# Kernel optimization log

Hardware: AMD Instinct MI355X
Metric: run time of the kernel (lower is better)

## Reference

```python
import jax, jax.numpy as jnp
import numpy as np

BEAM = 4
SOS = 1


def _gru_cell(x, h, Wih, Whh, bih, bhh):
    # x,h: [B,H]; Wih,Whh: [3H,H]; torch GRUCell math
    gi = x @ Wih.T + bih
    gh = h @ Whh.T + bhh
    ir, iz, inn = jnp.split(gi, 3, axis=-1)
    hr, hz, hn = jnp.split(gh, 3, axis=-1)
    r = jax.nn.sigmoid(ir + hr)
    z = jax.nn.sigmoid(iz + hz)
    n = jnp.tanh(inn + r * hn)
    return (1.0 - z) * n + z * h


def setup_inputs() -> dict:
    key = jax.random.key(0)
    V, H, S, L = 32000, 1024, 256, 48
    ks = jax.random.split(key, 10)
    p = lambda k, shape: (jax.random.normal(k, shape, jnp.float32) * 0.02)
    return {
        "input_seq": jax.random.randint(ks[0], (S, 1), 0, V),
        "input_length": S,
        "max_length": L,
        "emb": p(ks[1], (V, H)),
        "enc_Wih": p(ks[2], (3 * H, H)),
        "enc_Whh": p(ks[3], (3 * H, H)),
        "enc_bih": jnp.zeros((3 * H,), jnp.float32),
        "enc_bhh": jnp.zeros((3 * H,), jnp.float32),
        "dec_Wih": p(ks[4], (3 * H, H)),
        "dec_Whh": p(ks[5], (3 * H, H)),
        "dec_bih": jnp.zeros((3 * H,), jnp.float32),
        "dec_bhh": jnp.zeros((3 * H,), jnp.float32),
        "Wc": p(ks[6], (H, 2 * H)),
        "Wout": p(ks[7], (V, H)),
    }


def _beam_search(input_seq, max_length, emb, enc_Wih, enc_Whh, enc_bih, enc_bhh,
                 dec_Wih, dec_Whh, dec_bih, dec_bhh, Wc, Wout):
    H = emb.shape[1]
    # ---- encoder: single-layer GRU over [S] tokens ----
    seq_emb = emb[input_seq[:, 0]]  # [S,H]

    def enc_step(h, x):
        hn = _gru_cell(x[None, :], h, enc_Wih, enc_Whh, enc_bih, enc_bhh)
        return hn, hn[0]

    h0 = jnp.zeros((1, H), emb.dtype)
    h_final, enc_out = jax.lax.scan(enc_step, h0, seq_emb)  # enc_out: [S,H]

    # ---- beam state (all beams start from encoder final hidden, SOS token) ----
    h = jnp.tile(h_final, (BEAM, 1))            # [4,H]
    inputs = jnp.full((BEAM,), SOS, jnp.int32)  # [4]
    cum = jnp.zeros((BEAM,), emb.dtype)
    tokens = jnp.zeros((BEAM, max_length), jnp.int32)
    shist = jnp.zeros((BEAM, max_length), emb.dtype)

    def dec_step(carry, step):
        h, inputs, cum, tokens, shist = carry
        x = emb[inputs]                                     # [4,H]
        hnew = _gru_cell(x, h, dec_Wih, dec_Whh, dec_bih, dec_bhh)  # [4,H]
        # Luong dot attention over encoder outputs
        attn = jax.nn.softmax(jnp.einsum('sh,bh->bs', enc_out, hnew), axis=-1)
        ctx = attn @ enc_out                                # [4,H]
        concat = jnp.tanh(jnp.concatenate([hnew, ctx], axis=-1) @ Wc.T)
        logp = jax.nn.log_softmax(concat @ Wout.T, axis=-1)  # [4,V]
        tp, ti = jax.lax.top_k(logp, BEAM)                  # [4,4]
        # step 0: only beam 0 expands (all beams identical), as in original
        valid = jnp.where(step == 0, jnp.arange(BEAM) == 0,
                          jnp.ones((BEAM,), bool))
        cand = jnp.where(valid[:, None], cum[:, None] + tp, -jnp.inf).reshape(-1)
        sel_scores, sel = jax.lax.top_k(cand, BEAM)         # [4]
        bi = sel // BEAM   # parent beam index i
        jj = sel % BEAM    # topk column index j
        # Faithful to original bug: new hidden indexed by column j, not parent i
        new_h = hnew[jj]
        new_inputs = ti[bi, jj]
        step_scores = tp[bi, jj]
        new_tokens = tokens[bi].at[:, step].set(new_inputs)
        new_shist = shist[bi].at[:, step].set(step_scores)
        return (new_h, new_inputs, sel_scores, new_tokens, new_shist), None

    (h, inputs, cum, tokens, shist), _ = jax.lax.scan(
        dec_step, (h, inputs, cum, tokens, shist), jnp.arange(max_length))
    best = jnp.argmax(cum)  # all beams same length -> avg == cum ranking
    return tokens[best], shist[best]


def reference(input_seq, input_length, max_length, emb, enc_Wih, enc_Whh,
              enc_bih, enc_bhh, dec_Wih, dec_Whh, dec_bih, dec_bhh, Wc, Wout):
    # input_length: full sequence is used (original packs to input_length;
    # here input_length == seq_len)
    return _beam_search(input_seq, max_length, emb, enc_Wih, enc_Whh, enc_bih,
                        enc_bhh, dec_Wih, dec_Whh, dec_bih, dec_bhh, Wc, Wout)
```

## Files before the change

kernel.cpp:

```cpp
#include <hip/hip_runtime.h>
#include <hip/hip_bf16.h>

#define HDIM 1024
#define G3   3072
#define CHK  16
#define NEG_INF (-__builtin_inff())
#define EB   32

typedef unsigned short u16;
typedef unsigned int   u32;

__device__ __forceinline__ float bf2f(u32 h){ union{u32 u; float f;} t; t.u = h<<16; return t.f; }

__device__ __forceinline__ float wred_sum(float v){
  #pragma unroll
  for(int o=32;o;o>>=1) v += __shfl_xor(v,o,64);
  return v;
}
__device__ __forceinline__ float wred_max(float v){
  #pragma unroll
  for(int o=32;o;o>>=1) v = fmaxf(v,__shfl_xor(v,o,64));
  return v;
}

__device__ __forceinline__ void load16w(const void* W, long long eoff, int bf, float* x){
  if(bf){
    const uint4* q = (const uint4*)((const u16*)W + eoff);
    uint4 a = q[0], b = q[1];
    x[0]=bf2f(a.x&0xffffu); x[1]=bf2f(a.x>>16);
    x[2]=bf2f(a.y&0xffffu); x[3]=bf2f(a.y>>16);
    x[4]=bf2f(a.z&0xffffu); x[5]=bf2f(a.z>>16);
    x[6]=bf2f(a.w&0xffffu); x[7]=bf2f(a.w>>16);
    x[8]=bf2f(b.x&0xffffu); x[9]=bf2f(b.x>>16);
    x[10]=bf2f(b.y&0xffffu); x[11]=bf2f(b.y>>16);
    x[12]=bf2f(b.z&0xffffu); x[13]=bf2f(b.z>>16);
    x[14]=bf2f(b.w&0xffffu); x[15]=bf2f(b.w>>16);
  } else {
    const float4* q = (const float4*)((const float*)W + eoff);
    float4 A=q[0],B=q[1],C=q[2],D=q[3];
    x[0]=A.x;x[1]=A.y;x[2]=A.z;x[3]=A.w;
    x[4]=B.x;x[5]=B.y;x[6]=B.z;x[7]=B.w;
    x[8]=C.x;x[9]=C.y;x[10]=C.z;x[11]=C.w;
    x[12]=D.x;x[13]=D.y;x[14]=D.z;x[15]=D.w;
  }
}
__device__ __forceinline__ void load16f(const float* p, float* x){
  const float4* q=(const float4*)p;
  float4 A=q[0],B=q[1],C=q[2],D=q[3];
  x[0]=A.x;x[1]=A.y;x[2]=A.z;x[3]=A.w;
  x[4]=B.x;x[5]=B.y;x[6]=B.z;x[7]=B.w;
  x[8]=C.x;x[9]=C.y;x[10]=C.z;x[11]=C.w;
  x[12]=D.x;x[13]=D.y;x[14]=D.z;x[15]=D.w;
}
__device__ __forceinline__ float loadscal(const void* p, long long i, int bf){
  return bf ? bf2f(((const u16*)p)[i]) : ((const float*)p)[i];
}
__device__ __forceinline__ float sigf(float x){ return 1.f/(1.f+expf(-x)); }

__device__ __forceinline__ void dot4_accum(const float* w, const float xr[4][16], float a[4]){
  #pragma unroll
  for(int i=0;i<16;i++){
    a[0] += w[i]*xr[0][i];
    a[1] += w[i]*xr[1][i];
    a[2] += w[i]*xr[2][i];
    a[3] += w[i]*xr[3][i];
  }
}

__device__ __forceinline__ void insert4(float* v, int* ix, float nv, int ni){
  bool b3 = (nv>v[3]) || (nv==v[3] && ni<ix[3]);
  if(!b3) return;
  bool b2 = (nv>v[2]) || (nv==v[2] && ni<ix[2]);
  bool b1 = (nv>v[1]) || (nv==v[1] && ni<ix[1]);
  bool b0 = (nv>v[0]) || (nv==v[0] && ni<ix[0]);
  if(b0){ v[3]=v[2];ix[3]=ix[2]; v[2]=v[1];ix[2]=ix[1]; v[1]=v[0];ix[1]=ix[0]; v[0]=nv;ix[0]=ni; }
  else if(b1){ v[3]=v[2];ix[3]=ix[2]; v[2]=v[1];ix[2]=ix[1]; v[1]=nv;ix[1]=ni; }
  else if(b2){ v[3]=v[2];ix[3]=ix[2]; v[2]=nv;ix[2]=ni; }
  else { v[3]=nv; ix[3]=ni; }
}
__device__ __forceinline__ void merge4(const float* va, const int* ia, const float* vb, const int* ib, float* vo, int* io){
  int pa=0, pb=0;
  for(int k=0;k<4;k++){
    bool ta;
    if(pa>=4) ta=false;
    else if(pb>=4) ta=true;
    else ta = (va[pa]>vb[pb]) || (va[pa]==vb[pb] && ia[pa]<ib[pb]);
    if(ta){ vo[k]=va[pa]; io[k]=ia[pa]; pa++; }
    else  { vo[k]=vb[pb]; io[k]=ib[pb]; pb++; }
  }
}

__device__ __forceinline__ void gbar(int* cnt, int nblk, int it){
  __syncthreads();
  if(threadIdx.x==0){
    __hip_atomic_fetch_add(cnt, 1, __ATOMIC_ACQ_REL, __HIP_MEMORY_SCOPE_AGENT);
    int target = nblk*it;
    while(__hip_atomic_load(cnt, __ATOMIC_ACQUIRE, __HIP_MEMORY_SCOPE_AGENT) < target)
      __builtin_amdgcn_s_sleep(1);
  }
  __syncthreads();
  __builtin_amdgcn_fence(__ATOMIC_ACQUIRE, "agent");
}

__global__ __launch_bounds__(256) void k_probe(const u16* emb, int* flag, int* bar_cnt){
  __shared__ int cnt;
  if(threadIdx.x==0){ cnt=0; *bar_cnt=0; }
  __syncthreads();
  int c=0;
  for(int i=threadIdx.x;i<4096;i+=256){
    u32 e = (emb[i]>>7)&0xffu;
    if(e>=0x85u) c++;
  }
  atomicAdd(&cnt,c);
  __syncthreads();
  if(threadIdx.x==0) *flag = (cnt<100)?1:0;
}

__global__ __launch_bounds__(256) void k_enc_gi(const int* seq, const void* emb, const void* Wih,
                                                const void* bih, const int* flag, float* gi){
  int bf = *flag;
  int wg = blockIdx.x; int tg = wg>>3, rg = wg&7;
  int wave = threadIdx.x>>6, lane = threadIdx.x&63;
  int tok[4];
  #pragma unroll
  for(int j=0;j<4;j++) tok[j] = seq[tg*4+j];
  float xr[4][16];
  #pragma unroll
  for(int j=0;j<4;j++) load16w(emb, (long long)tok[j]*HDIM + lane*CHK, bf, xr[j]);
  for(int k=0;k<96;k++){
    int row = rg*384 + wave*96 + k;
    float w[16]; load16w(Wih, (long long)row*HDIM + lane*CHK, bf, w);
    float a[4]={0.f,0.f,0.f,0.f};
    dot4_accum(w, xr, a);
    float bias = loadscal(bih, row, bf);
    #pragma unroll
    for(int b=0;b<4;b++){
      float v = wred_sum(a[b]);
      if(lane==b) gi[(long long)(tg*4+b)*G3 + row] = v + bias;
    }
  }
}

__global__ __launch_bounds__(512,2) void k_enc_persist(const void* Whh, const void* bhh,
                                                       const int* flag, const float* gi,
                                                       float* enc_out, int S, int* bar_cnt){
  int bf = *flag;
  int wave = threadIdx.x>>6, lane = threadIdx.x&63;
  int dbase = blockIdx.x*32;
  __shared__ float gh_s[96];
  __shared__ float bhh_s[96];
  if(threadIdx.x<96){
    int rl = threadIdx.x;
    int row = (rl>>5)*HDIM + dbase + (rl&31);
    bhh_s[rl] = loadscal(bhh, row, bf);
  }
  float wreg[12][16];
  #pragma unroll
  for(int k=0;k<12;k++){
    int rl = wave*12 + k;
    int row = (rl>>5)*HDIM + dbase + (rl&31);
    load16w(Whh, (long long)row*HDIM + lane*CHK, bf, wreg[k]);
  }
  __syncthreads();

  for(int t=0;t<S;t++){
    if(t>0) gbar(bar_cnt, EB, t);
    float h[16];
    if(t>0){
      load16f(enc_out + (long long)(t-1)*HDIM + lane*CHK, h);
    } else {
      #pragma unroll
      for(int i=0;i<16;i++) h[i]=0.f;
    }
    #pragma unroll
    for(int k=0;k<12;k++){
      float a=0.f;
      #pragma unroll
      for(int i=0;i<16;i++) a += wreg[k][i]*h[i];
      a = wred_sum(a);
      if(lane==k) gh_s[wave*12+k] = a + bhh_s[wave*12+k];
    }
    __syncthreads();
    if(threadIdx.x<32){
      int d = threadIdx.x;
      int gd = dbase + d;
      const float* gir = gi + (long long)t*G3;
      float ir = gir[gd], iz = gir[HDIM+gd], in_ = gir[2*HDIM+gd];
      float hr = gh_s[d], hz = gh_s[32+d], hn = gh_s[64+d];
      float r = sigf(ir+hr);
      float z = sigf(iz+hz);
      float n = tanhf(in_ + r*hn);
      float hp = (t>0) ? enc_out[(long long)(t-1)*HDIM + gd] : 0.f;
      enc_out[(long long)t*HDIM + gd] = (1.f-z)*n + z*hp;
    }
  }
}

__global__ __launch_bounds__(256) void k_dec_init(const float* enc_out, int S, float* h_cur, float* cum,
                                                  int* cur_in, int* tokens, float* shist, int L){
  int t = threadIdx.x;
  const float* hf = enc_out + (long long)(S-1)*HDIM;
  for(int i=t;i<4*HDIM;i+=256) h_cur[i] = hf[i&(HDIM-1)];
  if(t<4){ cum[t]=0.f; cur_in[t]=1; }
  for(int i=t;i<4*L;i+=256){ tokens[i]=0; shist[i]=0.f; }
}

__global__ __launch_bounds__(256) void k_dec_gru(const void* emb, const void* Wih, const void* Whh,
                                                 const void* bih, const void* bhh, const int* flag,
                                                 const int* cur_in, const float* h_cur, float* hnew){
  int bf = *flag;
  __shared__ float gibuf[96], ghbuf[96];
  int wave = threadIdx.x>>6, lane = threadIdx.x&63;
  int base = blockIdx.x*8;
  float xr[4][16];
  int tok[4];
  #pragma unroll
  for(int b=0;b<4;b++) tok[b]=cur_in[b];
  #pragma unroll
  for(int b=0;b<4;b++) load16w(emb,(long long)tok[b]*HDIM+lane*CHK,bf,xr[b]);
  for(int k=0;k<6;k++){
    int idx = wave*6+k; int g = idx>>3, d = idx&7;
    int row = g*HDIM + base + d;
    float w[16]; load16w(Wih,(long long)row*HDIM+lane*CHK,bf,w);
    float a[4]={0.f,0.f,0.f,0.f};
    dot4_accum(w,xr,a);
    float bias = loadscal(bih,row,bf);
    #pragma unroll
    for(int b=0;b<4;b++){
      float v = wred_sum(a[b]);
      if(lane==b) gibuf[idx*4+b] = v + bias;
    }
  }
  #pragma unroll
  for(int b=0;b<4;b++) load16f(h_cur+(long long)b*HDIM+lane*CHK, xr[b]);
  for(int k=0;k<6;k++){
    int idx = wave*6+k; int g = idx>>3, d = idx&7;
    int row = g*HDIM + base + d;
    float w[16]; load16w(Whh,(long long)row*HDIM+lane*CHK,bf,w);
    float a[4]={0.f,0.f,0.f,0.f};
    dot4_accum(w,xr,a);
    float bias = loadscal(bhh,row,bf);
    #pragma unroll
    for(int b=0;b<4;b++){
      float v = wred_sum(a[b]);
      if(lane==b) ghbuf[idx*4+b] = v + bias;
    }
  }
  __syncthreads();
  if(threadIdx.x<32){
    int d = threadIdx.x&7, b = threadIdx.x>>3;
    float ir = gibuf[(0*8+d)*4+b], iz = gibuf[(1*8+d)*4+b], in_ = gibuf[(2*8+d)*4+b];
    float hr = ghbuf[(0*8+d)*4+b], hz = ghbuf[(1*8+d)*4+b], hn = ghbuf[(2*8+d)*4+b];
    float r = sigf(ir+hr);
    float z = sigf(iz+hz);
    float n = tanhf(in_ + r*hn);
    float h = h_cur[b*HDIM + base + d];
    hnew[b*HDIM + base + d] = (1.f-z)*n + z*h;
  }
}

__global__ __launch_bounds__(256) void k_dec_scores(const float* enc_out, const float* hnew, float* scores){
  int wave = threadIdx.x>>6, lane = threadIdx.x&63;
  float xr[4][16];
  #pragma unroll
  for(int b=0;b<4;b++) load16f(hnew+(long long)b*HDIM+lane*CHK, xr[b]);
  for(int k=0;k<4;k++){
    int s = (blockIdx.x*4+wave)*4+k;
    float w[16]; load16f(enc_out+(long long)s*HDIM+lane*CHK, w);
    float a[4]={0.f,0.f,0.f,0.f};
    dot4_accum(w,xr,a);
    #pragma unroll
    for(int b=0;b<4;b++){
      float v = wred_sum(a[b]);
      if(lane==b) scores[s*4+b] = v;
    }
  }
}

__global__ __launch_bounds__(256) void k_dec_attnctx(const float* enc_out, const float* scores_g,
                                                     float* ctx, int S){
  __shared__ float sc[256*4];
  int t = threadIdx.x;
  for(int i=t;i<S*4;i+=256) sc[i]=scores_g[i];
  __syncthreads();
  int wave = t>>6, lane = t&63;
  {
    int b = wave;
    float v[4];
    #pragma unroll
    for(int k=0;k<4;k++) v[k]=sc[(lane+64*k)*4+b];
    float m = fmaxf(fmaxf(v[0],v[1]),fmaxf(v[2],v[3]));
    m = wred_max(m);
    float e[4]; float ss=0.f;
    #pragma unroll
    for(int k=0;k<4;k++){ e[k]=expf(v[k]-m); ss+=e[k]; }
    ss = wred_sum(ss);
    #pragma unroll
    for(int k=0;k<4;k++) sc[(lane+64*k)*4+b] = e[k]/ss;
  }
  __syncthreads();
  int hl = t&127, bp = t>>7;
  int h = blockIdx.x*128 + hl;
  int b0 = bp*2;
  float a0=0.f, a1=0.f;
  for(int s=0;s<S;s++){
    float e = enc_out[(long long)s*HDIM + h];
    a0 += sc[s*4+b0]*e;
    a1 += sc[s*4+b0+1]*e;
  }
  ctx[b0*HDIM+h]=a0; ctx[(b0+1)*HDIM+h]=a1;
}

__global__ __launch_bounds__(256) void k_dec_wc(const void* Wc, const int* flag, const float* hnew,
                                                const float* ctx, float* concat){
  int bf = *flag;
  int wave = threadIdx.x>>6, lane = threadIdx.x&63;
  int r0 = blockIdx.x*16 + wave*4;
  float xr[4][16];
  #pragma unroll
  for(int b=0;b<4;b++) load16f(hnew+(long long)b*HDIM+lane*CHK, xr[b]);
  float acc[4][4];
  #pragma unroll
  for(int k=0;k<4;k++){
    #pragma unroll
    for(int b=0;b<4;b++) acc[k][b]=0.f;
  }
  #pragma unroll
  for(int k=0;k<4;k++){
    float w[16]; load16w(Wc,(long long)(r0+k)*2048 + lane*CHK, bf, w);
    #pragma unroll
    for(int i=0;i<16;i++){
      acc[k][0]+=w[i]*xr[0][i]; acc[k][1]+=w[i]*xr[1][i];
      acc[k][2]+=w[i]*xr[2][i]; acc[k][3]+=w[i]*xr[3][i];
    }
  }
  #pragma unroll
  for(int b=0;b<4;b++) load16f(ctx+(long long)b*HDIM+lane*CHK, xr[b]);
  #pragma unroll
  for(int k=0;k<4;k++){
    float w[16]; load16w(Wc,(long long)(r0+k)*2048 + 1024 + lane*CHK, bf, w);
    #pragma unroll
    for(int i=0;i<16;i++){
      acc[k][0]+=w[i]*xr[0][i]; acc[k][1]+=w[i]*xr[1][i];
      acc[k][2]+=w[i]*xr[2][i]; acc[k][3]+=w[i]*xr[3][i];
    }
  }
  #pragma unroll
  for(int k=0;k<4;k++){
    #pragma unroll
    for(int b=0;b<4;b++){
      float v = wred_sum(acc[k][b]);
      if(lane == k*4+b) concat[b*HDIM + r0 + k] = tanhf(v);
    }
  }
}

__global__ __launch_bounds__(512) void k_dec_logits(const void* Wout, const int* flag, const float* concat,
                                                    float* pm, float* ps, float* ptv, int* pti, int V){
  int bf = *flag;
  int wave = threadIdx.x>>6, lane = threadIdx.x&63;
  float xr[4][16];
  #pragma unroll
  for(int b=0;b<4;b++) load16f(concat+(long long)b*HDIM+lane*CHK, xr[b]);
  int wbase = blockIdx.x*125;
  int off  = (wave<5) ? wave*16 : 80 + (wave-5)*15;
  int cnt  = (wave<5) ? 16 : 15;
  float m[4], s[4], tv[4][4]; int ti_[4][4];
  #pragma unroll
  for(int b=0;b<4;b++){
    m[b]=NEG_INF; s[b]=0.f;
    #pragma unroll
    for(int j=0;j<4;j++){ tv[b][j]=NEG_INF; ti_[b][j]=0; }
  }
  for(int k=0;k<cnt;k++){
    int row = wbase + off + k;
    if(row>=V) break;
    float w[16]; load16w(Wout,(long long)row*HDIM+lane*CHK,bf,w);
    float a[4]={0.f,0.f,0.f,0.f};
    dot4_accum(w,xr,a);
    a[0]=wred_sum(a[0]); a[1]=wred_sum(a[1]); a[2]=wred_sum(a[2]); a[3]=wred_sum(a[3]);
    if(lane==0){
      #pragma unroll
      for(int b=0;b<4;b++){
        float v = a[b];
        if(v>m[b]){ s[b]=s[b]*expf(m[b]-v)+1.f; m[b]=v; }
        else s[b] += expf(v-m[b]);
        insert4(tv[b], ti_[b], v, row);
      }
    }
  }
  __shared__ float lm[32], lssum[32], ltv[128]; __shared__ int lti[128];
  if(lane==0){
    #pragma unroll
    for(int b=0;b<4;b++){
      lm[wave*4+b]=m[b]; lssum[wave*4+b]=s[b];
      #pragma unroll
      for(int j=0;j<4;j++){ ltv[(wave*4+b)*4+j]=tv[b][j]; lti[(wave*4+b)*4+j]=ti_[b][j]; }
    }
  }
  __syncthreads();
  if(threadIdx.x==0){
    for(int b=0;b<4;b++){
      float M=NEG_INF;
      for(int w=0;w<8;w++) M=fmaxf(M,lm[w*4+b]);
      float S=0.f;
      for(int w=0;w<8;w++) S += lssum[w*4+b]*expf(lm[w*4+b]-M);
      float cv[4]; int ci[4];
      for(int j=0;j<4;j++){ cv[j]=ltv[(0*4+b)*4+j]; ci[j]=lti[(0*4+b)*4+j]; }
      for(int w=1;w<8;w++){
        float vo[4]; int io[4];
        merge4(cv,ci,&ltv[(w*4+b)*4],&lti[(w*4+b)*4],vo,io);
        for(int j=0;j<4;j++){ cv[j]=vo[j]; ci[j]=io[j]; }
      }
      pm[blockIdx.x*4+b]=M; ps[blockIdx.x*4+b]=S;
      for(int j=0;j<4;j++){ ptv[(blockIdx.x*4+b)*4+j]=cv[j]; pti[(blockIdx.x*4+b)*4+j]=ci[j]; }
    }
  }
}

__global__ __launch_bounds__(256) void k_dec_finalize(const float* pm, const float* ps, const float* ptv,
                                                      const int* pti, const float* hnew, float* h_cur,
                                                      float* cum, int* cur_in, int* tokens, float* shist,
                                                      int step, int L, const int* flag, void* dout){
  __shared__ float red[256];
  __shared__ float tpv[4][4]; __shared__ int tpi[4][4];
  __shared__ float logZ[4];
  __shared__ float mtv[256*4]; __shared__ int mti[256*4];
  __shared__ int l_bi[4], l_jj[4], l_tok[4]; __shared__ float l_ss[4], l_cum[4];
  __shared__ int otok[4*64]; __shared__ float oshi[4*64];
  __shared__ int bbest;
  int t = threadIdx.x;

  for(int b=0;b<4;b++){
    float v = pm[t*4+b];
    red[t]=v; __syncthreads();
    for(int st=128;st;st>>=1){ if(t<st) red[t]=fmaxf(red[t],red[t+st]); __syncthreads(); }
    float M = red[0]; __syncthreads();
    red[t] = ps[t*4+b]*expf(v-M); __syncthreads();
    for(int st=128;st;st>>=1){ if(t<st) red[t]+=red[t+st]; __syncthreads(); }
    if(t==0) logZ[b]=M+logf(red[0]);
    __syncthreads();
  }
  for(int b=0;b<4;b++){
    for(int j=0;j<4;j++){ mtv[t*4+j]=ptv[(t*4+b)*4+j]; mti[t*4+j]=pti[(t*4+b)*4+j]; }
    __syncthreads();
    for(int st=1; st<256; st<<=1){
      if((t & (2*st-1))==0 && t+st<256){
        float vo[4]; int io[4];
        merge4(&mtv[t*4], &mti[t*4], &mtv[(t+st)*4], &mti[(t+st)*4], vo, io);
        for(int j=0;j<4;j++){ mtv[t*4+j]=vo[j]; mti[t*4+j]=io[j]; }
      }
      __syncthreads();
    }
    if(t<4){ tpv[b][t]=mtv[t]-logZ[b]; tpi[b][t]=mti[t]; }
    __syncthreads();
  }
  if(t==0){
    float oc[4];
    for(int b=0;b<4;b++) oc[b]=cum[b];
    float cand[16];
    for(int b=0;b<4;b++)
      for(int j=0;j<4;j++){
        bool valid = (step>0)||(b==0);
        cand[b*4+j] = valid ? oc[b]+tpv[b][j] : NEG_INF;
      }
    bool used[16];
    for(int i=0;i<16;i++) used[i]=false;
    for(int q=0;q<4;q++){
      int best=0; float bv=NEG_INF;
      for(int i=0;i<16;i++){ if(!used[i] && cand[i]>bv){ bv=cand[i]; best=i; } }
      used[best]=true;
      int bi = best>>2, jj = best&3;
      l_bi[q]=bi; l_jj[q]=jj; l_tok[q]=tpi[bi][jj]; l_ss[q]=tpv[bi][jj]; l_cum[q]=bv;
    }
  }
  __syncthreads();
  for(int i=t;i<4*L;i+=256){ otok[i]=tokens[i]; oshi[i]=shist[i]; }
  __syncthreads();
  for(int i=t;i<4*L;i+=256){
    int q=i/L, c=i%L;
    int src=l_bi[q];
    tokens[i] = (c==step)? l_tok[q] : otok[src*L+c];
    shist[i]  = (c==step)? l_ss[q]  : oshi[src*L+c];
  }
  if(t<4){ cum[t]=l_cum[t]; cur_in[t]=l_tok[t]; }
  for(int i=t;i<4*HDIM;i+=256){
    int q=i>>10;
    h_cur[i] = hnew[l_jj[q]*HDIM + (i&(HDIM-1))];
  }
  if(step==L-1){
    if(t==0){
      int bb=0; float bv=l_cum[0];
      for(int b=1;b<4;b++) if(l_cum[b]>bv){ bv=l_cum[b]; bb=b; }
      bbest=bb;
    }
    __syncthreads();
    int bb=bbest; int bf=*flag;
    for(int c=t;c<L;c+=256){
      float tokv = (float)((c==step)? l_tok[bb] : otok[l_bi[bb]*L+c]);
      float shv  = (c==step)? l_ss[bb] : oshi[l_bi[bb]*L+c];
      if(bf){
        __hip_bfloat16* o = (__hip_bfloat16*)dout;
        o[c]   = __float2bfloat16(tokv);
        o[L+c] = __float2bfloat16(shv);
      } else {
        float* o = (float*)dout;
        o[c]   = tokv;
        o[L+c] = shv;
      }
    }
  }
}

extern "C" void kernel_launch(void* const* d_in, const int* in_sizes, int n_in,
                              void* d_out, int out_size, void* d_ws, size_t ws_size,
                              hipStream_t stream) {
  const int* seq   = (const int*)d_in[0];
  const void* emb  = d_in[3];
  const void* eWih = d_in[4]; const void* eWhh = d_in[5];
  const void* ebih = d_in[6]; const void* ebhh = d_in[7];
  const void* dWih = d_in[8]; const void* dWhh = d_in[9];
  const void* dbih = d_in[10]; const void* dbhh = d_in[11];
  const void* Wc   = d_in[12]; const void* Wout = d_in[13];

  int S = in_sizes[0];
  int L = out_size/2;
  int V = in_sizes[13]/HDIM;

  char* p = (char*)d_ws;
  auto carve = [&](size_t bytes)->void* {
    void* r = (void*)p;
    p += (bytes + 255) & ~(size_t)255;
    return r;
  };
  int*   flag    = (int*)  carve(4);
  int*   bar_cnt = (int*)  carve(4);
  float* gi_enc  = (float*)carve((size_t)S*G3*4);
  float* enc_out = (float*)carve((size_t)S*HDIM*4);
  float* h_cur   = (float*)carve(4*HDIM*4);
  float* hnew    = (float*)carve(4*HDIM*4);
  float* scoresb = (float*)carve((size_t)S*4*4);
  float* ctx     = (float*)carve(4*HDIM*4);
  float* concat  = (float*)carve(4*HDIM*4);
  float* pm      = (float*)carve(256*4*4);
  float* ps      = (float*)carve(256*4*4);
  float* ptv     = (float*)carve(256*16*4);
  int*   pti     = (int*)  carve(256*16*4);
  float* cum     = (float*)carve(4*4);
  int*   cur_in  = (int*)  carve(4*4);
  int*   tokens  = (int*)  carve(4*L*4);
  float* shist   = (float*)carve(4*L*4);

  k_probe<<<1,256,0,stream>>>((const u16*)emb, flag, bar_cnt);
  k_enc_gi<<<(S/4)*8,256,0,stream>>>(seq, emb, eWih, ebih, flag, gi_enc);
  k_enc_persist<<<EB,512,0,stream>>>(eWhh, ebhh, flag, gi_enc, enc_out, S, bar_cnt);
  k_dec_init<<<1,256,0,stream>>>(enc_out, S, h_cur, cum, cur_in, tokens, shist, L);
  for(int st=0;st<L;st++){
    k_dec_gru<<<128,256,0,stream>>>(emb, dWih, dWhh, dbih, dbhh, flag, cur_in, h_cur, hnew);
    k_dec_scores<<<16,256,0,stream>>>(enc_out, hnew, scoresb);
    k_dec_attnctx<<<8,256,0,stream>>>(enc_out, scoresb, ctx, S);
    k_dec_wc<<<64,256,0,stream>>>(Wc, flag, hnew, ctx, concat);
    k_dec_logits<<<256,512,0,stream>>>(Wout, flag, concat, pm, ps, ptv, pti, V);
    k_dec_finalize<<<1,256,0,stream>>>(pm, ps, ptv, pti, hnew, h_cur, cum, cur_in,
                                       tokens, shist, st, L, flag, d_out);
  }
}
```

Before: 9.962 ms.

## Fuse decoder step kernels into one persistent kernel with hierarchical grid barrier

Replaces the six per-step decoder kernel launches (288 launches over 48 steps) with a single persistent kernel of 256 blocks. The stages are separated by a two-level grid barrier built from per-group atomic counters and a release flag. Beam state (tokens, score history, cumulative scores) now lives in block 0's shared memory instead of global memory. The goal is to remove launch overhead and inter-kernel gaps. The cost is spin-wait barriers, which assume all 256 blocks are co-resident, plus extra work imbalance across blocks.

```diff
diff --git a/kernel.cpp b/kernel.cpp
--- a/kernel.cpp
+++ b/kernel.cpp
@@ -6,6 +6,7 @@
 #define CHK  16
 #define NEG_INF (-__builtin_inff())
 #define EB   32
+#define DB   256
 
 typedef unsigned short u16;
 typedef unsigned int   u32;
@@ -102,9 +103,32 @@
   __builtin_amdgcn_fence(__ATOMIC_ACQUIRE, "agent");
 }
 
-__global__ __launch_bounds__(256) void k_probe(const u16* emb, int* flag, int* bar_cnt){
+__device__ __forceinline__ void gbar2(int* cnts, int* rel, int it){
+  __syncthreads();
+  if(threadIdx.x==0){
+    int g = blockIdx.x & 7;
+    __hip_atomic_fetch_add(&cnts[g*64], 1, __ATOMIC_ACQ_REL, __HIP_MEMORY_SCOPE_AGENT);
+    if(blockIdx.x==0){
+      #pragma unroll
+      for(int g2=0; g2<8; ++g2){
+        while(__hip_atomic_load(&cnts[g2*64], __ATOMIC_ACQUIRE, __HIP_MEMORY_SCOPE_AGENT) < 32*it)
+          __builtin_amdgcn_s_sleep(1);
+      }
+      __hip_atomic_store(rel, it, __ATOMIC_RELEASE, __HIP_MEMORY_SCOPE_AGENT);
+    } else {
+      while(__hip_atomic_load(rel, __ATOMIC_ACQUIRE, __HIP_MEMORY_SCOPE_AGENT) < it)
+        __builtin_amdgcn_s_sleep(1);
+    }
+  }
+  __syncthreads();
+  __builtin_amdgcn_fence(__ATOMIC_ACQUIRE, "agent");
+}
+
+__global__ __launch_bounds__(256) void k_probe(const u16* emb, int* flag, int* bar_cnt,
+                                               int* dcnts, int* drel){
   __shared__ int cnt;
-  if(threadIdx.x==0){ cnt=0; *bar_cnt=0; }
+  if(threadIdx.x==0){ cnt=0; *bar_cnt=0; *drel=0; }
+  for(int i=threadIdx.x;i<512;i+=256) dcnts[i]=0;
   __syncthreads();
   int c=0;
   for(int i=threadIdx.x;i<4096;i+=256){
@@ -196,319 +220,310 @@
   }
 }
 
-__global__ __launch_bounds__(256) void k_dec_init(const float* enc_out, int S, float* h_cur, float* cum,
-                                                  int* cur_in, int* tokens, float* shist, int L){
+__global__ __launch_bounds__(512,2) void k_dec_persist(
+    const void* emb, const void* Wih, const void* Whh,
+    const void* bih, const void* bhh, const void* Wc, const void* Wout,
+    const int* flag, const float* enc_out, int S, int L, int V,
+    float* h_cur, float* hnew, float* scoresb, float* ctx, float* concat,
+    float* pm, float* ps, float* ptv, int* pti, int* cur_in,
+    int* cnts, int* rel, void* dout)
+{
+  int bf = *flag;
   int t = threadIdx.x;
-  const float* hf = enc_out + (long long)(S-1)*HDIM;
-  for(int i=t;i<4*HDIM;i+=256) h_cur[i] = hf[i&(HDIM-1)];
-  if(t<4){ cum[t]=0.f; cur_in[t]=1; }
-  for(int i=t;i<4*L;i+=256){ tokens[i]=0; shist[i]=0.f; }
-}
-
-__global__ __launch_bounds__(256) void k_dec_gru(const void* emb, const void* Wih, const void* Whh,
-                                                 const void* bih, const void* bhh, const int* flag,
-                                                 const int* cur_in, const float* h_cur, float* hnew){
-  int bf = *flag;
-  __shared__ float gibuf[96], ghbuf[96];
-  int wave = threadIdx.x>>6, lane = threadIdx.x&63;
-  int base = blockIdx.x*8;
-  float xr[4][16];
-  int tok[4];
-  #pragma unroll
-  for(int b=0;b<4;b++) tok[b]=cur_in[b];
-  #pragma unroll
-  for(int b=0;b<4;b++) load16w(emb,(long long)tok[b]*HDIM+lane*CHK,bf,xr[b]);
-  for(int k=0;k<6;k++){
-    int idx = wave*6+k; int g = idx>>3, d = idx&7;
-    int row = g*HDIM + base + d;
-    float w[16]; load16w(Wih,(long long)row*HDIM+lane*CHK,bf,w);
-    float a[4]={0.f,0.f,0.f,0.f};
-    dot4_accum(w,xr,a);
-    float bias = loadscal(bih,row,bf);
-    #pragma unroll
-    for(int b=0;b<4;b++){
-      float v = wred_sum(a[b]);
-      if(lane==b) gibuf[idx*4+b] = v + bias;
-    }
-  }
-  #pragma unroll
-  for(int b=0;b<4;b++) load16f(h_cur+(long long)b*HDIM+lane*CHK, xr[b]);
-  for(int k=0;k<6;k++){
-    int idx = wave*6+k; int g = idx>>3, d = idx&7;
-    int row = g*HDIM + base + d;
-    float w[16]; load16w(Whh,(long long)row*HDIM+lane*CHK,bf,w);
-    float a[4]={0.f,0.f,0.f,0.f};
-    dot4_accum(w,xr,a);
-    float bias = loadscal(bhh,row,bf);
-    #pragma unroll
-    for(int b=0;b<4;b++){
-      float v = wred_sum(a[b]);
-      if(lane==b) ghbuf[idx*4+b] = v + bias;
-    }
-  }
-  __syncthreads();
-  if(threadIdx.x<32){
-    int d = threadIdx.x&7, b = threadIdx.x>>3;
-    float ir = gibuf[(0*8+d)*4+b], iz = gibuf[(1*8+d)*4+b], in_ = gibuf[(2*8+d)*4+b];
-    float hr = ghbuf[(0*8+d)*4+b], hz = ghbuf[(1*8+d)*4+b], hn = ghbuf[(2*8+d)*4+b];
-    float r = sigf(ir+hr);
-    float z = sigf(iz+hz);
-    float n = tanhf(in_ + r*hn);
-    float h = h_cur[b*HDIM + base + d];
-    hnew[b*HDIM + base + d] = (1.f-z)*n + z*h;
-  }
-}
-
-__global__ __launch_bounds__(256) void k_dec_scores(const float* enc_out, const float* hnew, float* scores){
-  int wave = threadIdx.x>>6, lane = threadIdx.x&63;
-  float xr[4][16];
-  #pragma unroll
-  for(int b=0;b<4;b++) load16f(hnew+(long long)b*HDIM+lane*CHK, xr[b]);
-  for(int k=0;k<4;k++){
-    int s = (blockIdx.x*4+wave)*4+k;
-    float w[16]; load16f(enc_out+(long long)s*HDIM+lane*CHK, w);
-    float a[4]={0.f,0.f,0.f,0.f};
-    dot4_accum(w,xr,a);
-    #pragma unroll
-    for(int b=0;b<4;b++){
-      float v = wred_sum(a[b]);
-      if(lane==b) scores[s*4+b] = v;
-    }
-  }
-}
-
-__global__ __launch_bounds__(256) void k_dec_attnctx(const float* enc_out, const float* scores_g,
-                                                     float* ctx, int S){
-  __shared__ float sc[256*4];
-  int t = threadIdx.x;
-  for(int i=t;i<S*4;i+=256) sc[i]=scores_g[i];
-  __syncthreads();
   int wave = t>>6, lane = t&63;
-  {
-    int b = wave;
-    float v[4];
-    #pragma unroll
-    for(int k=0;k<4;k++) v[k]=sc[(lane+64*k)*4+b];
-    float m = fmaxf(fmaxf(v[0],v[1]),fmaxf(v[2],v[3]));
-    m = wred_max(m);
-    float e[4]; float ss=0.f;
-    #pragma unroll
-    for(int k=0;k<4;k++){ e[k]=expf(v[k]-m); ss+=e[k]; }
-    ss = wred_sum(ss);
-    #pragma unroll
-    for(int k=0;k<4;k++) sc[(lane+64*k)*4+b] = e[k]/ss;
-  }
-  __syncthreads();
-  int hl = t&127, bp = t>>7;
-  int h = blockIdx.x*128 + hl;
-  int b0 = bp*2;
-  float a0=0.f, a1=0.f;
-  for(int s=0;s<S;s++){
-    float e = enc_out[(long long)s*HDIM + h];
-    a0 += sc[s*4+b0]*e;
-    a1 += sc[s*4+b0+1]*e;
-  }
-  ctx[b0*HDIM+h]=a0; ctx[(b0+1)*HDIM+h]=a1;
-}
-
-__global__ __launch_bounds__(256) void k_dec_wc(const void* Wc, const int* flag, const float* hnew,
-                                                const float* ctx, float* concat){
-  int bf = *flag;
-  int wave = threadIdx.x>>6, lane = threadIdx.x&63;
-  int r0 = blockIdx.x*16 + wave*4;
-  float xr[4][16];
-  #pragma unroll
-  for(int b=0;b<4;b++) load16f(hnew+(long long)b*HDIM+lane*CHK, xr[b]);
-  float acc[4][4];
-  #pragma unroll
-  for(int k=0;k<4;k++){
-    #pragma unroll
-    for(int b=0;b<4;b++) acc[k][b]=0.f;
-  }
-  #pragma unroll
-  for(int k=0;k<4;k++){
-    float w[16]; load16w(Wc,(long long)(r0+k)*2048 + lane*CHK, bf, w);
-    #pragma unroll
-    for(int i=0;i<16;i++){
-      acc[k][0]+=w[i]*xr[0][i]; acc[k][1]+=w[i]*xr[1][i];
-      acc[k][2]+=w[i]*xr[2][i]; acc[k][3]+=w[i]*xr[3][i];
-    }
-  }
-  #pragma unroll
-  for(int b=0;b<4;b++) load16f(ctx+(long long)b*HDIM+lane*CHK, xr[b]);
-  #pragma unroll
-  for(int k=0;k<4;k++){
-    float w[16]; load16w(Wc,(long long)(r0+k)*2048 + 1024 + lane*CHK, bf, w);
-    #pragma unroll
-    for(int i=0;i<16;i++){
-      acc[k][0]+=w[i]*xr[0][i]; acc[k][1]+=w[i]*xr[1][i];
-      acc[k][2]+=w[i]*xr[2][i]; acc[k][3]+=w[i]*xr[3][i];
-    }
-  }
-  #pragma unroll
-  for(int k=0;k<4;k++){
-    #pragma unroll
-    for(int b=0;b<4;b++){
-      float v = wred_sum(acc[k][b]);
-      if(lane == k*4+b) concat[b*HDIM + r0 + k] = tanhf(v);
-    }
-  }
-}
-
-__global__ __launch_bounds__(512) void k_dec_logits(const void* Wout, const int* flag, const float* concat,
-                                                    float* pm, float* ps, float* ptv, int* pti, int V){
-  int bf = *flag;
-  int wave = threadIdx.x>>6, lane = threadIdx.x&63;
-  float xr[4][16];
-  #pragma unroll
-  for(int b=0;b<4;b++) load16f(concat+(long long)b*HDIM+lane*CHK, xr[b]);
-  int wbase = blockIdx.x*125;
-  int off  = (wave<5) ? wave*16 : 80 + (wave-5)*15;
-  int cnt  = (wave<5) ? 16 : 15;
-  float m[4], s[4], tv[4][4]; int ti_[4][4];
-  #pragma unroll
-  for(int b=0;b<4;b++){
-    m[b]=NEG_INF; s[b]=0.f;
-    #pragma unroll
-    for(int j=0;j<4;j++){ tv[b][j]=NEG_INF; ti_[b][j]=0; }
-  }
-  for(int k=0;k<cnt;k++){
-    int row = wbase + off + k;
-    if(row>=V) break;
-    float w[16]; load16w(Wout,(long long)row*HDIM+lane*CHK,bf,w);
-    float a[4]={0.f,0.f,0.f,0.f};
-    dot4_accum(w,xr,a);
-    a[0]=wred_sum(a[0]); a[1]=wred_sum(a[1]); a[2]=wred_sum(a[2]); a[3]=wred_sum(a[3]);
-    if(lane==0){
+  int blk = blockIdx.x;
+
+  __shared__ float gibuf[48], ghbuf[48];
+  __shared__ float pbuf[1024];
+  __shared__ float lm[32], lssum[32], ltv[128]; __shared__ int lti[128];
+  __shared__ float red[512];
+  __shared__ float mtv[512*4]; __shared__ int mti[512*4];
+  __shared__ float tpv[4][4]; __shared__ int tpi[4][4];
+  __shared__ float logZ[4];
+  __shared__ int l_bi[4], l_jj[4], l_tok[4]; __shared__ float l_ss[4], l_cum[4];
+  __shared__ float cum_l[4];
+  __shared__ int   tok_l[4*64]; __shared__ float shi_l[4*64];
+  __shared__ int   otok[4*64];  __shared__ float oshi[4*64];
+  __shared__ int bbest;
+
+  if(blk==0){
+    const float* hf = enc_out + (long long)(S-1)*HDIM;
+    for(int i=t;i<4*HDIM;i+=512) h_cur[i] = hf[i&(HDIM-1)];
+    if(t<4){ cum_l[t]=0.f; cur_in[t]=1; }
+    for(int i=t;i<4*64;i+=512){ tok_l[i]=0; shi_l[i]=0.f; }
+  }
+  int bit = 0;
+  gbar2(cnts, rel, ++bit);
+
+  for(int st=0; st<L; ++st){
+    {
+      int base = blk*4;
+      float xr[4][16];
+      if(wave<4){
+        int tok[4];
+        #pragma unroll
+        for(int b=0;b<4;b++) tok[b]=cur_in[b];
+        #pragma unroll
+        for(int b=0;b<4;b++) load16w(emb,(long long)tok[b]*HDIM+lane*CHK,bf,xr[b]);
+        #pragma unroll
+        for(int k=0;k<3;k++){
+          int idx = wave*3+k; int g=idx>>2, d=idx&3;
+          int row = g*HDIM + base + d;
+          float w[16]; load16w(Wih,(long long)row*HDIM+lane*CHK,bf,w);
+          float a[4]={0.f,0.f,0.f,0.f};
+          dot4_accum(w,xr,a);
+          float bias = loadscal(bih,row,bf);
+          #pragma unroll
+          for(int b=0;b<4;b++){
+            float v = wred_sum(a[b]);
+            if(lane==b) gibuf[idx*4+b] = v + bias;
+          }
+        }
+      } else {
+        #pragma unroll
+        for(int b=0;b<4;b++) load16f(h_cur+(long long)b*HDIM+lane*CHK, xr[b]);
+        #pragma unroll
+        for(int k=0;k<3;k++){
+          int idx = (wave-4)*3+k; int g=idx>>2, d=idx&3;
+          int row = g*HDIM + base + d;
+          float w[16]; load16w(Whh,(long long)row*HDIM+lane*CHK,bf,w);
+          float a[4]={0.f,0.f,0.f,0.f};
+          dot4_accum(w,xr,a);
+          float bias = loadscal(bhh,row,bf);
+          #pragma unroll
+          for(int b=0;b<4;b++){
+            float v = wred_sum(a[b]);
+            if(lane==b) ghbuf[idx*4+b] = v + bias;
+          }
+        }
+      }
+      __syncthreads();
+      if(t<16){
+        int d=t&3, b=t>>2;
+        float ir=gibuf[(0*4+d)*4+b], iz=gibuf[(1*4+d)*4+b], in_=gibuf[(2*4+d)*4+b];
+        float hr=ghbuf[(0*4+d)*4+b], hz=ghbuf[(1*4+d)*4+b], hn=ghbuf[(2*4+d)*4+b];
+        float r = sigf(ir+hr);
+        float z = sigf(iz+hz);
+        float n = tanhf(in_ + r*hn);
+        float h = h_cur[b*HDIM + base + d];
+        hnew[b*HDIM + base + d] = (1.f-z)*n + z*h;
+      }
+    }
+    gbar2(cnts, rel, ++bit);
+
+    if(blk < S && wave < 4){
+      float x[16]; load16f(hnew+(long long)wave*HDIM+lane*CHK, x);
+      float e[16]; load16f(enc_out+(long long)blk*HDIM+lane*CHK, e);
+      float a=0.f;
+      #pragma unroll
+      for(int i=0;i<16;i++) a += x[i]*e[i];
+      a = wred_sum(a);
+      if(lane==0) scoresb[blk*4+wave] = a;
+    }
+    gbar2(cnts, rel, ++bit);
+
+    if(blk < 8){
+      pbuf[t]       = scoresb[t];
+      pbuf[t+512]   = scoresb[t+512];
+      __syncthreads();
+      if(wave<4){
+        int b = wave;
+        float v[4];
+        #pragma unroll
+        for(int k=0;k<4;k++) v[k]=pbuf[(lane+64*k)*4+b];
+        float m = fmaxf(fmaxf(v[0],v[1]),fmaxf(v[2],v[3]));
+        m = wred_max(m);
+        float e[4]; float ss=0.f;
+        #pragma unroll
+        for(int k=0;k<4;k++){ e[k]=expf(v[k]-m); ss+=e[k]; }
+        ss = wred_sum(ss);
+        #pragma unroll
+        for(int k=0;k<4;k++) pbuf[(lane+64*k)*4+b] = e[k]/ss;
+      }
+      __syncthreads();
+      int hl = t>>2, b = t&3;
+      int h = blk*128 + hl;
+      float a = 0.f;
+      #pragma unroll 8
+      for(int s=0;s<256;s++) a += pbuf[s*4+b]*enc_out[(long long)s*HDIM + h];
+      ctx[b*HDIM+h] = a;
+    }
+    gbar2(cnts, rel, ++bit);
+
+    {
+      int r = blk*4 + (wave>>1);
+      int b0 = (wave&1)*2;
+      float acc0=0.f, acc1=0.f;
+      {
+        float w[16]; load16w(Wc,(long long)r*2048 + lane*CHK, bf, w);
+        float x0[16], x1[16];
+        load16f(hnew+(long long)b0*HDIM+lane*CHK, x0);
+        load16f(hnew+(long long)(b0+1)*HDIM+lane*CHK, x1);
+        #pragma unroll
+        for(int i=0;i<16;i++){ acc0+=w[i]*x0[i]; acc1+=w[i]*x1[i]; }
+      }
+      {
+        float w[16]; load16w(Wc,(long long)r*2048 + 1024 + lane*CHK, bf, w);
+        float x0[16], x1[16];
+        load16f(ctx+(long long)b0*HDIM+lane*CHK, x0);
+        load16f(ctx+(long long)(b0+1)*HDIM+lane*CHK, x1);
+        #pragma unroll
+        for(int i=0;i<16;i++){ acc0+=w[i]*x0[i]; acc1+=w[i]*x1[i]; }
+      }
+      acc0 = wred_sum(acc0); acc1 = wred_sum(acc1);
+      if(lane==0){
+        concat[b0*HDIM + r]     = tanhf(acc0);
+        concat[(b0+1)*HDIM + r] = tanhf(acc1);
+      }
+    }
+    gbar2(cnts, rel, ++bit);
+
+    {
+      float xr[4][16];
+      #pragma unroll
+      for(int b=0;b<4;b++) load16f(concat+(long long)b*HDIM+lane*CHK, xr[b]);
+      int wbase = blk*125;
+      int off  = (wave<5) ? wave*16 : 80 + (wave-5)*15;
+      int cnt  = (wave<5) ? 16 : 15;
+      float m[4], s[4], tv[4][4]; int ti_[4][4];
       #pragma unroll
       for(int b=0;b<4;b++){
-        float v = a[b];
-        if(v>m[b]){ s[b]=s[b]*expf(m[b]-v)+1.f; m[b]=v; }
-        else s[b] += expf(v-m[b]);
-        insert4(tv[b], ti_[b], v, row);
-      }
-    }
-  }
-  __shared__ float lm[32], lssum[32], ltv[128]; __shared__ int lti[128];
-  if(lane==0){
-    #pragma unroll
-    for(int b=0;b<4;b++){
-      lm[wave*4+b]=m[b]; lssum[wave*4+b]=s[b];
-      #pragma unroll
-      for(int j=0;j<4;j++){ ltv[(wave*4+b)*4+j]=tv[b][j]; lti[(wave*4+b)*4+j]=ti_[b][j]; }
-    }
-  }
-  __syncthreads();
-  if(threadIdx.x==0){
-    for(int b=0;b<4;b++){
-      float M=NEG_INF;
-      for(int w=0;w<8;w++) M=fmaxf(M,lm[w*4+b]);
-      float S=0.f;
-      for(int w=0;w<8;w++) S += lssum[w*4+b]*expf(lm[w*4+b]-M);
-      float cv[4]; int ci[4];
-      for(int j=0;j<4;j++){ cv[j]=ltv[(0*4+b)*4+j]; ci[j]=lti[(0*4+b)*4+j]; }
-      for(int w=1;w<8;w++){
-        float vo[4]; int io[4];
-        merge4(cv,ci,&ltv[(w*4+b)*4],&lti[(w*4+b)*4],vo,io);
-        for(int j=0;j<4;j++){ cv[j]=vo[j]; ci[j]=io[j]; }
-      }
-      pm[blockIdx.x*4+b]=M; ps[blockIdx.x*4+b]=S;
-      for(int j=0;j<4;j++){ ptv[(blockIdx.x*4+b)*4+j]=cv[j]; pti[(blockIdx.x*4+b)*4+j]=ci[j]; }
-    }
-  }
-}
-
-__global__ __launch_bounds__(256) void k_dec_finalize(const float* pm, const float* ps, const float* ptv,
-                                                      const int* pti, const float* hnew, float* h_cur,
-                                                      float* cum, int* cur_in, int* tokens, float* shist,
-                                                      int step, int L, const int* flag, void* dout){
-  __shared__ float red[256];
-  __shared__ float tpv[4][4]; __shared__ int tpi[4][4];
-  __shared__ float logZ[4];
-  __shared__ float mtv[256*4]; __shared__ int mti[256*4];
-  __shared__ int l_bi[4], l_jj[4], l_tok[4]; __shared__ float l_ss[4], l_cum[4];
-  __shared__ int otok[4*64]; __shared__ float oshi[4*64];
-  __shared__ int bbest;
-  int t = threadIdx.x;
-
-  for(int b=0;b<4;b++){
-    float v = pm[t*4+b];
-    red[t]=v; __syncthreads();
-    for(int st=128;st;st>>=1){ if(t<st) red[t]=fmaxf(red[t],red[t+st]); __syncthreads(); }
-    float M = red[0]; __syncthreads();
-    red[t] = ps[t*4+b]*expf(v-M); __syncthreads();
-    for(int st=128;st;st>>=1){ if(t<st) red[t]+=red[t+st]; __syncthreads(); }
-    if(t==0) logZ[b]=M+logf(red[0]);
-    __syncthreads();
-  }
-  for(int b=0;b<4;b++){
-    for(int j=0;j<4;j++){ mtv[t*4+j]=ptv[(t*4+b)*4+j]; mti[t*4+j]=pti[(t*4+b)*4+j]; }
-    __syncthreads();
-    for(int st=1; st<256; st<<=1){
-      if((t & (2*st-1))==0 && t+st<256){
-        float vo[4]; int io[4];
-        merge4(&mtv[t*4], &mti[t*4], &mtv[(t+st)*4], &mti[(t+st)*4], vo, io);
-        for(int j=0;j<4;j++){ mtv[t*4+j]=vo[j]; mti[t*4+j]=io[j]; }
+        m[b]=NEG_INF; s[b]=0.f;
+        #pragma unroll
+        for(int j=0;j<4;j++){ tv[b][j]=NEG_INF; ti_[b][j]=0; }
+      }
+      for(int k=0;k<cnt;k++){
+        int row = wbase + off + k;
+        if(row>=V) break;
+        float w[16]; load16w(Wout,(long long)row*HDIM+lane*CHK,bf,w);
+        float a[4]={0.f,0.f,0.f,0.f};
+        dot4_accum(w,xr,a);
+        a[0]=wred_sum(a[0]); a[1]=wred_sum(a[1]); a[2]=wred_sum(a[2]); a[3]=wred_sum(a[3]);
+        if(lane==0){
+          #pragma unroll
+          for(int b=0;b<4;b++){
+            float v = a[b];
+            if(v>m[b]){ s[b]=s[b]*expf(m[b]-v)+1.f; m[b]=v; }
+            else s[b] += expf(v-m[b]);
+            insert4(tv[b], ti_[b], v, row);
+          }
+        }
+      }
+      if(lane==0){
+        #pragma unroll
+        for(int b=0;b<4;b++){
+          lm[wave*4+b]=m[b]; lssum[wave*4+b]=s[b];
+          #pragma unroll
+          for(int j=0;j<4;j++){ ltv[(wave*4+b)*4+j]=tv[b][j]; lti[(wave*4+b)*4+j]=ti_[b][j]; }
+        }
       }
       __syncthreads();
-    }
-    if(t<4){ tpv[b][t]=mtv[t]-logZ[b]; tpi[b][t]=mti[t]; }
-    __syncthreads();
-  }
-  if(t==0){
-    float oc[4];
-    for(int b=0;b<4;b++) oc[b]=cum[b];
-    float cand[16];
-    for(int b=0;b<4;b++)
-      for(int j=0;j<4;j++){
-        bool valid = (step>0)||(b==0);
-        cand[b*4+j] = valid ? oc[b]+tpv[b][j] : NEG_INF;
-      }
-    bool used[16];
-    for(int i=0;i<16;i++) used[i]=false;
-    for(int q=0;q<4;q++){
-      int best=0; float bv=NEG_INF;
-      for(int i=0;i<16;i++){ if(!used[i] && cand[i]>bv){ bv=cand[i]; best=i; } }
-      used[best]=true;
-      int bi = best>>2, jj = best&3;
-      l_bi[q]=bi; l_jj[q]=jj; l_tok[q]=tpi[bi][jj]; l_ss[q]=tpv[bi][jj]; l_cum[q]=bv;
-    }
-  }
-  __syncthreads();
-  for(int i=t;i<4*L;i+=256){ otok[i]=tokens[i]; oshi[i]=shist[i]; }
-  __syncthreads();
-  for(int i=t;i<4*L;i+=256){
-    int q=i/L, c=i%L;
-    int src=l_bi[q];
-    tokens[i] = (c==step)? l_tok[q] : otok[src*L+c];
-    shist[i]  = (c==step)? l_ss[q]  : oshi[src*L+c];
-  }
-  if(t<4){ cum[t]=l_cum[t]; cur_in[t]=l_tok[t]; }
-  for(int i=t;i<4*HDIM;i+=256){
-    int q=i>>10;
-    h_cur[i] = hnew[l_jj[q]*HDIM + (i&(HDIM-1))];
-  }
-  if(step==L-1){
-    if(t==0){
-      int bb=0; float bv=l_cum[0];
-      for(int b=1;b<4;b++) if(l_cum[b]>bv){ bv=l_cum[b]; bb=b; }
-      bbest=bb;
-    }
-    __syncthreads();
-    int bb=bbest; int bf=*flag;
-    for(int c=t;c<L;c+=256){
-      float tokv = (float)((c==step)? l_tok[bb] : otok[l_bi[bb]*L+c]);
-      float shv  = (c==step)? l_ss[bb] : oshi[l_bi[bb]*L+c];
-      if(bf){
-        __hip_bfloat16* o = (__hip_bfloat16*)dout;
-        o[c]   = __float2bfloat16(tokv);
-        o[L+c] = __float2bfloat16(shv);
-      } else {
-        float* o = (float*)dout;
-        o[c]   = tokv;
-        o[L+c] = shv;
-      }
-    }
+      if(t==0){
+        for(int b=0;b<4;b++){
+          float M=NEG_INF;
+          for(int w=0;w<8;w++) M=fmaxf(M,lm[w*4+b]);
+          float Ssum=0.f;
+          for(int w=0;w<8;w++) Ssum += lssum[w*4+b]*expf(lm[w*4+b]-M);
+          float cv[4]; int ci[4];
+          for(int j=0;j<4;j++){ cv[j]=ltv[(0*4+b)*4+j]; ci[j]=lti[(0*4+b)*4+j]; }
+          for(int w=1;w<8;w++){
+            float vo[4]; int io[4];
+            merge4(cv,ci,&ltv[(w*4+b)*4],&lti[(w*4+b)*4],vo,io);
+            for(int j=0;j<4;j++){ cv[j]=vo[j]; ci[j]=io[j]; }
+          }
+          pm[blk*4+b]=M; ps[blk*4+b]=Ssum;
+          for(int j=0;j<4;j++){ ptv[(blk*4+b)*4+j]=cv[j]; pti[(blk*4+b)*4+j]=ci[j]; }
+        }
+      }
+    }
+    gbar2(cnts, rel, ++bit);
+
+    if(blk==0){
+      for(int b=0;b<4;b++){
+        float v = (t<256) ? pm[t*4+b] : NEG_INF;
+        red[t]=v; __syncthreads();
+        for(int sp=256;sp;sp>>=1){ if(t<sp) red[t]=fmaxf(red[t],red[t+sp]); __syncthreads(); }
+        float M = red[0]; __syncthreads();
+        red[t] = (t<256) ? ps[t*4+b]*expf(v-M) : 0.f; __syncthreads();
+        for(int sp=256;sp;sp>>=1){ if(t<sp) red[t]+=red[t+sp]; __syncthreads(); }
+        if(t==0) logZ[b]=M+logf(red[0]);
+        __syncthreads();
+      }
+      for(int b=0;b<4;b++){
+        if(t<256){
+          for(int j=0;j<4;j++){ mtv[t*4+j]=ptv[(t*4+b)*4+j]; mti[t*4+j]=pti[(t*4+b)*4+j]; }
+        } else {
+          for(int j=0;j<4;j++){ mtv[t*4+j]=NEG_INF; mti[t*4+j]=0; }
+        }
+        __syncthreads();
+        for(int sp=1; sp<512; sp<<=1){
+          if((t & (2*sp-1))==0 && t+sp<512){
+            float vo[4]; int io[4];
+            merge4(&mtv[t*4], &mti[t*4], &mtv[(t+sp)*4], &mti[(t+sp)*4], vo, io);
+            for(int j=0;j<4;j++){ mtv[t*4+j]=vo[j]; mti[t*4+j]=io[j]; }
+          }
+          __syncthreads();
+        }
+        if(t<4){ tpv[b][t]=mtv[t]-logZ[b]; tpi[b][t]=mti[t]; }
+        __syncthreads();
+      }
+      if(t==0){
+        float oc[4];
+        for(int b=0;b<4;b++) oc[b]=cum_l[b];
+        float cand[16];
+        for(int b=0;b<4;b++)
+          for(int j=0;j<4;j++){
+            bool valid = (st>0)||(b==0);
+            cand[b*4+j] = valid ? oc[b]+tpv[b][j] : NEG_INF;
+          }
+        bool used[16];
+        for(int i=0;i<16;i++) used[i]=false;
+        for(int q=0;q<4;q++){
+          int best=0; float bv=NEG_INF;
+          for(int i=0;i<16;i++){ if(!used[i] && cand[i]>bv){ bv=cand[i]; best=i; } }
+          used[best]=true;
+          int bi = best>>2, jj = best&3;
+          l_bi[q]=bi; l_jj[q]=jj; l_tok[q]=tpi[bi][jj]; l_ss[q]=tpv[bi][jj]; l_cum[q]=bv;
+        }
+      }
+      __syncthreads();
+      for(int i=t;i<4*L;i+=512){ otok[i]=tok_l[i]; oshi[i]=shi_l[i]; }
+      __syncthreads();
+      for(int i=t;i<4*L;i+=512){
+        int q=i/L, c=i%L;
+        int src=l_bi[q];
+        tok_l[i] = (c==st)? l_tok[q] : otok[src*L+c];
+        shi_l[i] = (c==st)? l_ss[q]  : oshi[src*L+c];
+      }
+      if(t<4){ cum_l[t]=l_cum[t]; cur_in[t]=l_tok[t]; }
+      for(int i=t;i<4*HDIM;i+=512){
+        int q=i>>10;
+        h_cur[i] = hnew[l_jj[q]*HDIM + (i&(HDIM-1))];
+      }
+      if(st==L-1){
+        if(t==0){
+          int bb=0; float bv=l_cum[0];
+          for(int b=1;b<4;b++) if(l_cum[b]>bv){ bv=l_cum[b]; bb=b; }
+          bbest=bb;
+        }
+        __syncthreads();
+        int bb=bbest;
+        for(int c=t;c<L;c+=512){
+          float tokv = (float)((c==st)? l_tok[bb] : otok[l_bi[bb]*L+c]);
+          float shv  = (c==st)? l_ss[bb] : oshi[l_bi[bb]*L+c];
+          if(bf){
+            __hip_bfloat16* o = (__hip_bfloat16*)dout;
+            o[c]   = __float2bfloat16(tokv);
+            o[L+c] = __float2bfloat16(shv);
+          } else {
+            float* o = (float*)dout;
+            o[c]   = tokv;
+            o[L+c] = shv;
+          }
+        }
+      }
+    }
+    gbar2(cnts, rel, ++bit);
   }
 }
 
@@ -535,6 +550,8 @@
   };
   int*   flag    = (int*)  carve(4);
   int*   bar_cnt = (int*)  carve(4);
+  int*   dcnts   = (int*)  carve(512*4);
+  int*   drel    = (int*)  carve(64*4);
   float* gi_enc  = (float*)carve((size_t)S*G3*4);
   float* enc_out = (float*)carve((size_t)S*HDIM*4);
   float* h_cur   = (float*)carve(4*HDIM*4);
@@ -546,22 +563,14 @@
   float* ps      = (float*)carve(256*4*4);
   float* ptv     = (float*)carve(256*16*4);
   int*   pti     = (int*)  carve(256*16*4);
-  float* cum     = (float*)carve(4*4);
   int*   cur_in  = (int*)  carve(4*4);
-  int*   tokens  = (int*)  carve(4*L*4);
-  float* shist   = (float*)carve(4*L*4);
-
-  k_probe<<<1,256,0,stream>>>((const u16*)emb, flag, bar_cnt);
+
+  k_probe<<<1,256,0,stream>>>((const u16*)emb, flag, bar_cnt, dcnts, drel);
   k_enc_gi<<<(S/4)*8,256,0,stream>>>(seq, emb, eWih, ebih, flag, gi_enc);
   k_enc_persist<<<EB,512,0,stream>>>(eWhh, ebhh, flag, gi_enc, enc_out, S, bar_cnt);
-  k_dec_init<<<1,256,0,stream>>>(enc_out, S, h_cur, cum, cur_in, tokens, shist, L);
-  for(int st=0;st<L;st++){
-    k_dec_gru<<<128,256,0,stream>>>(emb, dWih, dWhh, dbih, dbhh, flag, cur_in, h_cur, hnew);
-    k_dec_scores<<<16,256,0,stream>>>(enc_out, hnew, scoresb);
-    k_dec_attnctx<<<8,256,0,stream>>>(enc_out, scoresb, ctx, S);
-    k_dec_wc<<<64,256,0,stream>>>(Wc, flag, hnew, ctx, concat);
-    k_dec_logits<<<256,512,0,stream>>>(Wout, flag, concat, pm, ps, ptv, pti, V);
-    k_dec_finalize<<<1,256,0,stream>>>(pm, ps, ptv, pti, hnew, h_cur, cum, cur_in,
-                                       tokens, shist, st, L, flag, d_out);
-  }
-}
+  k_dec_persist<<<DB,512,0,stream>>>(emb, dWih, dWhh, dbih, dbhh, Wc, Wout,
+                                     flag, enc_out, S, L, V,
+                                     h_cur, hnew, scoresb, ctx, concat,
+                                     pm, ps, ptv, pti, cur_in,
+                                     dcnts, drel, d_out);
+}
```

After: 32.68 ms. +228.1%, slower.
